# Optimization experiments

Hardware: AMD Instinct MI355X
Metric: run time of the kernel (lower is better)

The kernel has to match this reference:

```python
import jax, jax.numpy as jnp
import numpy as np

N_UNITS = 1024
D_K = 64
B, S = 4, 2048
NEG = 1.0e9


def setup_inputs() -> dict:
    key = jax.random.key(0)
    ks = jax.random.split(key, 11)
    k = float(np.sqrt(1.0 / N_UNITS))
    u = lambda kk, shape: jax.random.uniform(kk, shape, jnp.float32, -k, k)
    Q = jax.random.normal(ks[0], (B, S, N_UNITS), jnp.float32)
    K = jax.random.normal(ks[1], (B, S, N_UNITS), jnp.float32)
    V = jax.random.normal(ks[2], (B, S, N_UNITS), jnp.float32)
    mask = jax.random.randint(ks[3], (B, S, S), 0, 2, jnp.int32)
    return {
        "Q": Q, "K": K, "V": V, "mask": mask,
        "Wq_w": u(ks[4], (D_K, N_UNITS)), "Wq_b": u(ks[5], (D_K,)),
        "Wk_w": u(ks[6], (D_K, N_UNITS)), "Wk_b": u(ks[7], (D_K,)),
        "Wv_w": u(ks[8], (D_K, N_UNITS)), "Wv_b": u(ks[9], (D_K,)),
    }


def reference(Q, K, V, mask, Wq_w, Wq_b, Wk_w, Wk_b, Wv_w, Wv_b):
    # Linear projections (torch Linear: x @ W.T + b)
    Q_ = jnp.einsum('bsu,du->bsd', Q, Wq_w) + Wq_b  # [B,S,D_K]
    K_ = jnp.einsum('bsu,du->bsd', K, Wk_w) + Wk_b
    V_ = jnp.einsum('bsu,du->bsd', V, Wv_w) + Wv_b
    scores = jnp.einsum('bid,bjd->bij', Q_, K_) / jnp.sqrt(jnp.float32(D_K))
    m = mask.astype(jnp.float32)
    # custom multiplicative-additive mask: scores*mask - 1e9*(1-mask)
    masked = scores * m - NEG * (1.0 - m)
    attn = jax.nn.softmax(masked, axis=-1)
    # dropout p=0.0 -> identity
    return jnp.einsum('bij,bjd->bid', attn, V_)
```

## Files before the change

kernel.cpp:

```cpp
#include <hip/hip_runtime.h>
#include <stdint.h>

#define S_ 2048

typedef __bf16 bf16x8 __attribute__((ext_vector_type(8)));
typedef float f32x4 __attribute__((ext_vector_type(4)));
typedef unsigned int u32x4 __attribute__((ext_vector_type(4)));

union FragU { u32x4 u; bf16x8 v; unsigned short s[8]; };

__device__ __forceinline__ unsigned short f2bf(float f) {
    unsigned int u = __builtin_bit_cast(unsigned int, f);
    u += 0x7fffu + ((u >> 16) & 1u);
    return (unsigned short)(u >> 16);
}
__device__ __forceinline__ unsigned int pk2(float a, float b) {
    return (unsigned int)f2bf(a) | ((unsigned int)f2bf(b) << 16);
}
__device__ __forceinline__ void gl_lds16(const void* g, void* l) {
    __builtin_amdgcn_global_load_lds(
        (const __attribute__((address_space(1))) unsigned int*)g,
        (__attribute__((address_space(3))) unsigned int*)l, 16, 0, 0);
}

__global__ __launch_bounds__(256) void cvt_w_kernel(
    const float* __restrict__ wq, const float* __restrict__ wk,
    const float* __restrict__ wv, u32x4* __restrict__ Wt4)
{
    const int lane = threadIdx.x & 63;
    const int lm = lane & 15, quad = lane >> 4;
    const int f = blockIdx.x * 4 + (threadIdx.x >> 6);
    const int mat = f >> 7, cg = (f >> 5) & 3, s = f & 31;
    const float* W = (mat == 0) ? wq : (mat == 1) ? wk : wv;
    const float* src = W + (cg * 16 + lm) * 1024 + s * 32 + quad * 8;
    float4 a = *(const float4*)(src);
    float4 b = *(const float4*)(src + 4);
    FragU o;
    o.u[0] = pk2(a.x, a.y); o.u[1] = pk2(a.z, a.w);
    o.u[2] = pk2(b.x, b.y); o.u[3] = pk2(b.z, b.w);
    Wt4[f * 64 + lane] = o.u;
}

__global__ __launch_bounds__(256, 2) void proj_mask_kernel(
    const float* __restrict__ Q, const float* __restrict__ K, const float* __restrict__ V,
    const u32x4* __restrict__ Wt4,
    const float* __restrict__ Bq, const float* __restrict__ Bk, const float* __restrict__ Bv,
    const int* __restrict__ mask,
    unsigned short* __restrict__ Qb, unsigned short* __restrict__ Kb,
    unsigned short* __restrict__ Vf,
    unsigned long long* __restrict__ bits)
{
    const int tid = threadIdx.x;
    const int w = tid >> 6, lane = tid & 63;
    const int g = blockIdx.x / 7, j = blockIdx.x % 7;

    __shared__ __align__(16) float Xs[16][1028];

    if (j >= 3) {
        const int wid = (g * 4 + (j - 3)) * 4 + w;
        const int* p = mask + wid * 2048 + lane;
        int mm[32];
        #pragma unroll
        for (int t = 0; t < 32; ++t) mm[t] = p[t * 64];
        #pragma unroll
        for (int t = 0; t < 32; ++t) {
            unsigned long long bb = __ballot(mm[t] != 0);
            if (lane == 0) bits[wid * 32 + t] = bb;
        }
        return;
    }

    const int lm = lane & 15, quad = lane >> 4;
    const int mat = j;
    const int row0 = g * 16;

    const float* X    = (mat == 0) ? Q  : (mat == 1) ? K  : V;
    const float* Bias = (mat == 0) ? Bq : (mat == 1) ? Bk : Bv;

    #pragma unroll
    for (int i = 0; i < 16; ++i) {
        const int r = w * 4 + (i >> 2);
        const int qd = i & 3;
        gl_lds16(X + (row0 + r) * 1024 + qd * 256 + lane * 4, &Xs[r][qd * 256]);
    }
    __syncthreads();

    f32x4 acc = {0.f, 0.f, 0.f, 0.f};
    const u32x4* wfrag = Wt4 + (mat * 128 + w * 32) * 64 + lane;
    #pragma unroll 8
    for (int s = 0; s < 32; ++s) {
        f32x4 a0 = *(const f32x4*)&Xs[lm][s * 32 + quad * 8];
        f32x4 a1 = *(const f32x4*)&Xs[lm][s * 32 + quad * 8 + 4];
        FragU af, bfr;
        af.u[0] = pk2(a0[0], a0[1]); af.u[1] = pk2(a0[2], a0[3]);
        af.u[2] = pk2(a1[0], a1[1]); af.u[3] = pk2(a1[2], a1[3]);
        bfr.u = wfrag[s * 64];
        acc = __builtin_amdgcn_mfma_f32_16x16x32_bf16(af.v, bfr.v, acc, 0, 0, 0);
    }

    const int col = w * 16 + lm;
    const float bias = Bias[col];
    if (mat == 2) {
        const int seq0 = row0 + quad * 4;
        const int b_ = seq0 >> 11;
        const int s = seq0 & 2047;
        const int sb = s >> 5, s32 = s & 31;
        const int fq = s32 >> 3, j0 = s32 & 7;
        ushort4 vv;
        unsigned short* vs = (unsigned short*)&vv;
        #pragma unroll
        for (int r = 0; r < 4; ++r) vs[r] = f2bf(acc[r] + bias);
        char* dst = (char*)Vf + ((b_ * 64 + sb) * 4 + w) * 1024
                    + (fq * 16 + lm) * 16 + j0 * 2;
        *(ushort4*)dst = vv;
    } else {
        unsigned short* dst = (mat == 0) ? Qb : Kb;
        #pragma unroll
        for (int r = 0; r < 4; ++r)
            dst[(row0 + quad * 4 + r) * 64 + col] = f2bf(acc[r] + bias);
    }
}

__global__ __launch_bounds__(512) void attn_kernel(
    const unsigned short* __restrict__ Qb, const unsigned short* __restrict__ Kb,
    const u32x4* __restrict__ Vf4, const unsigned long long* __restrict__ bits,
    float* __restrict__ out)
{
    const int tid = threadIdx.x;
    const int w = tid >> 6, lane = tid & 63;
    const int lm = lane & 15, quad = lane >> 4;
    const int q0 = blockIdx.x * 16;
    const int b = blockIdx.y;

    __shared__ unsigned long long Mb[16][32];
    __shared__ unsigned short Plds[8][16 * 72];
    __shared__ float Olds[8][1024];
    __shared__ float llds[8][16];

    {
        const int p = tid >> 5, kw = tid & 31;
        Mb[p][kw] = bits[(b * 2048 + q0 + p) * 32 + kw];
    }

    FragU qf0, qf1;
    const unsigned short* qptr = Qb + (b * 2048 + q0 + lm) * 64 + quad * 8;
    qf0.u = *(const u32x4*)qptr;
    qf1.u = *(const u32x4*)(qptr + 32);

    f32x4 o[4];
    #pragma unroll
    for (int dt = 0; dt < 4; ++dt) { f32x4 z = {0.f,0.f,0.f,0.f}; o[dt] = z; }
    float lsum[4] = {0.f, 0.f, 0.f, 0.f};

    const unsigned short* kbase = Kb + b * 2048 * 64;
    const u32x4* vbase = Vf4 + (b * 64) * 4 * 64;

    __syncthreads();

    #pragma unroll
    for (int iter = 0; iter < 4; ++iter) {
        const int k0 = w * 256 + iter * 64;
        const int kw = k0 >> 6;

        f32x4 sc[4];
        #pragma unroll
        for (int ct = 0; ct < 4; ++ct) {
            const unsigned short* kptr = kbase + (k0 + ct * 16 + lm) * 64 + quad * 8;
            FragU kf0, kf1;
            kf0.u = *(const u32x4*)kptr;
            kf1.u = *(const u32x4*)(kptr + 32);
            f32x4 a = {0.f,0.f,0.f,0.f};
            a = __builtin_amdgcn_mfma_f32_16x16x32_bf16(qf0.v, kf0.v, a, 0, 0, 0);
            a = __builtin_amdgcn_mfma_f32_16x16x32_bf16(qf1.v, kf1.v, a, 0, 0, 0);
            sc[ct] = a;
        }

        unsigned long long mb[4];
        #pragma unroll
        for (int r = 0; r < 4; ++r) mb[r] = Mb[quad * 4 + r][kw];

        #pragma unroll
        for (int ct = 0; ct < 4; ++ct) {
            #pragma unroll
            for (int r = 0; r < 4; ++r) {
                float p = ((mb[r] >> (ct * 16 + lm)) & 1ull)
                          ? __expf(sc[ct][r] * 0.125f) : 0.f;
                sc[ct][r] = p;
                lsum[r] += p;
            }
        }

        #pragma unroll
        for (int ct = 0; ct < 4; ++ct)
            #pragma unroll
            for (int r = 0; r < 4; ++r)
                Plds[w][(quad * 4 + r) * 72 + ct * 16 + lm] = f2bf(sc[ct][r]);

        #pragma unroll
        for (int ks = 0; ks < 2; ++ks) {
            FragU pf;
            pf.u = *(const u32x4*)&Plds[w][lm * 72 + ks * 32 + quad * 8];
            const int sb = (k0 >> 5) + ks;
            #pragma unroll
            for (int dt = 0; dt < 4; ++dt) {
                FragU vf;
                vf.u = vbase[(sb * 4 + dt) * 64 + lane];
                o[dt] = __builtin_amdgcn_mfma_f32_16x16x32_bf16(pf.v, vf.v, o[dt], 0, 0, 0);
            }
        }
    }

    #pragma unroll
    for (int r = 0; r < 4; ++r)
        #pragma unroll
        for (int off = 1; off <= 8; off <<= 1)
            lsum[r] += __shfl_xor(lsum[r], off, 64);

    #pragma unroll
    for (int dt = 0; dt < 4; ++dt)
        #pragma unroll
        for (int r = 0; r < 4; ++r)
            Olds[w][(quad * 4 + r) * 64 + dt * 16 + lm] = o[dt][r];
    if (lm == 0)
        #pragma unroll
        for (int r = 0; r < 4; ++r) llds[w][quad * 4 + r] = lsum[r];
    __syncthreads();

    #pragma unroll
    for (int i = 0; i < 2; ++i) {
        int e = i * 512 + tid;
        int q = e >> 6, d = e & 63;
        float L = 0.f, val = 0.f;
        #pragma unroll
        for (int ww = 0; ww < 8; ++ww) {
            L   += llds[ww][q];
            val += Olds[ww][q * 64 + d];
        }
        out[(b * 2048 + q0 + q) * 64 + d] = val / L;
    }
}

extern "C" void kernel_launch(void* const* d_in, const int* in_sizes, int n_in,
                              void* d_out, int out_size, void* d_ws, size_t ws_size,
                              hipStream_t stream) {
    const float* Q   = (const float*)d_in[0];
    const float* K   = (const float*)d_in[1];
    const float* V   = (const float*)d_in[2];
    const int* mask  = (const int*)d_in[3];
    const float* Wq  = (const float*)d_in[4];
    const float* bq  = (const float*)d_in[5];
    const float* Wk  = (const float*)d_in[6];
    const float* bk  = (const float*)d_in[7];
    const float* Wv  = (const float*)d_in[8];
    const float* bv  = (const float*)d_in[9];
    float* out = (float*)d_out;

    char* ws = (char*)d_ws;
    unsigned short* Qb = (unsigned short*)(ws);
    unsigned short* Kb = (unsigned short*)(ws + (1u << 20));
    unsigned short* Vf = (unsigned short*)(ws + (2u << 20));
    u32x4* Wt4 = (u32x4*)(ws + (3u << 20));
    unsigned long long* bits = (unsigned long long*)(ws + (4u << 20));

    hipLaunchKernelGGL(cvt_w_kernel, dim3(96), dim3(256), 0, stream, Wq, Wk, Wv, Wt4);
    hipLaunchKernelGGL(proj_mask_kernel, dim3(3584), dim3(256), 0, stream,
                       Q, K, V, Wt4, bq, bk, bv, mask, Qb, Kb, Vf, bits);
    hipLaunchKernelGGL(attn_kernel, dim3(128, 4), dim3(512), 0, stream,
                       Qb, Kb, (const u32x4*)Vf, bits, out);
}
```

Before: 215.1 us.

## Store K in MFMA fragment layout and process 32 queries per attention block

The projection kernel now writes K directly in the per-lane MFMA fragment order, so the attention kernel fetches each K fragment with one coalesced 16-byte load per lane instead of strided row loads. The attention kernel now handles 32 query rows per block, with waves split into two query groups and four key groups, each covering 512 keys. Each loaded K/V tile now serves two query tiles across the block, and the grid is halved. In exchange there are fewer blocks (256) and a longer per-wave loop, which may reduce latency hiding.

```diff
diff --git a/kernel.cpp b/kernel.cpp
--- a/kernel.cpp
+++ b/kernel.cpp
@@ -46,7 +46,7 @@
     const u32x4* __restrict__ Wt4,
     const float* __restrict__ Bq, const float* __restrict__ Bk, const float* __restrict__ Bv,
     const int* __restrict__ mask,
-    unsigned short* __restrict__ Qb, unsigned short* __restrict__ Kb,
+    unsigned short* __restrict__ Qb, unsigned short* __restrict__ Kf,
     unsigned short* __restrict__ Vf,
     unsigned long long* __restrict__ bits)
 {
@@ -100,7 +100,17 @@
 
     const int col = w * 16 + lm;
     const float bias = Bias[col];
-    if (mat == 2) {
+    if (mat == 0) {
+        #pragma unroll
+        for (int r = 0; r < 4; ++r)
+            Qb[(row0 + quad * 4 + r) * 64 + col] = f2bf(acc[r] + bias);
+    } else if (mat == 1) {
+        const int qp = (w & 1) * 2 + (lm >> 3);
+        unsigned short* base = Kf + ((unsigned)(g * 2 + (w >> 1)) * 64 + qp * 16 + quad * 4) * 8 + (lm & 7);
+        #pragma unroll
+        for (int r = 0; r < 4; ++r)
+            base[r * 8] = f2bf(acc[r] + bias);
+    } else {
         const int seq0 = row0 + quad * 4;
         const int b_ = seq0 >> 11;
         const int s = seq0 & 2047;
@@ -113,37 +123,36 @@
         char* dst = (char*)Vf + ((b_ * 64 + sb) * 4 + w) * 1024
                     + (fq * 16 + lm) * 16 + j0 * 2;
         *(ushort4*)dst = vv;
-    } else {
-        unsigned short* dst = (mat == 0) ? Qb : Kb;
-        #pragma unroll
-        for (int r = 0; r < 4; ++r)
-            dst[(row0 + quad * 4 + r) * 64 + col] = f2bf(acc[r] + bias);
     }
 }
 
 __global__ __launch_bounds__(512) void attn_kernel(
-    const unsigned short* __restrict__ Qb, const unsigned short* __restrict__ Kb,
+    const unsigned short* __restrict__ Qb, const u32x4* __restrict__ Kf4,
     const u32x4* __restrict__ Vf4, const unsigned long long* __restrict__ bits,
     float* __restrict__ out)
 {
     const int tid = threadIdx.x;
     const int w = tid >> 6, lane = tid & 63;
     const int lm = lane & 15, quad = lane >> 4;
-    const int q0 = blockIdx.x * 16;
+    const int qg = w & 1, kg = w >> 1;
+    const int q0 = blockIdx.x * 32;
     const int b = blockIdx.y;
 
-    __shared__ unsigned long long Mb[16][32];
+    __shared__ unsigned long long Mb[32][32];
     __shared__ unsigned short Plds[8][16 * 72];
-    __shared__ float Olds[8][1024];
-    __shared__ float llds[8][16];
+    __shared__ float Olds[4][32 * 64];
+    __shared__ float llds[4][32];
 
     {
-        const int p = tid >> 5, kw = tid & 31;
-        Mb[p][kw] = bits[(b * 2048 + q0 + p) * 32 + kw];
+        const int e0 = tid * 2;
+        const int p = e0 >> 5, kw = e0 & 31;
+        const unsigned long long* src = bits + (b * 2048 + q0 + p) * 32 + kw;
+        Mb[p][kw] = src[0];
+        Mb[p][kw + 1] = src[1];
     }
 
     FragU qf0, qf1;
-    const unsigned short* qptr = Qb + (b * 2048 + q0 + lm) * 64 + quad * 8;
+    const unsigned short* qptr = Qb + (b * 2048 + q0 + qg * 16 + lm) * 64 + quad * 8;
     qf0.u = *(const u32x4*)qptr;
     qf1.u = *(const u32x4*)(qptr + 32);
 
@@ -152,23 +161,23 @@
     for (int dt = 0; dt < 4; ++dt) { f32x4 z = {0.f,0.f,0.f,0.f}; o[dt] = z; }
     float lsum[4] = {0.f, 0.f, 0.f, 0.f};
 
-    const unsigned short* kbase = Kb + b * 2048 * 64;
+    const u32x4* kfb = Kf4 + (b * 128) * 2 * 64;
     const u32x4* vbase = Vf4 + (b * 64) * 4 * 64;
 
     __syncthreads();
 
-    #pragma unroll
-    for (int iter = 0; iter < 4; ++iter) {
-        const int k0 = w * 256 + iter * 64;
-        const int kw = k0 >> 6;
+    #pragma unroll 4
+    for (int iter = 0; iter < 8; ++iter) {
+        const int k0 = kg * 512 + iter * 64;
+        const int kw = kg * 8 + iter;
 
         f32x4 sc[4];
         #pragma unroll
         for (int ct = 0; ct < 4; ++ct) {
-            const unsigned short* kptr = kbase + (k0 + ct * 16 + lm) * 64 + quad * 8;
+            const int kt = (k0 >> 4) + ct;
             FragU kf0, kf1;
-            kf0.u = *(const u32x4*)kptr;
-            kf1.u = *(const u32x4*)(kptr + 32);
+            kf0.u = kfb[(kt * 2 + 0) * 64 + lane];
+            kf1.u = kfb[(kt * 2 + 1) * 64 + lane];
             f32x4 a = {0.f,0.f,0.f,0.f};
             a = __builtin_amdgcn_mfma_f32_16x16x32_bf16(qf0.v, kf0.v, a, 0, 0, 0);
             a = __builtin_amdgcn_mfma_f32_16x16x32_bf16(qf1.v, kf1.v, a, 0, 0, 0);
@@ -177,7 +186,7 @@
 
         unsigned long long mb[4];
         #pragma unroll
-        for (int r = 0; r < 4; ++r) mb[r] = Mb[quad * 4 + r][kw];
+        for (int r = 0; r < 4; ++r) mb[r] = Mb[qg * 16 + quad * 4 + r][kw];
 
         #pragma unroll
         for (int ct = 0; ct < 4; ++ct) {
@@ -220,21 +229,21 @@
     for (int dt = 0; dt < 4; ++dt)
         #pragma unroll
         for (int r = 0; r < 4; ++r)
-            Olds[w][(quad * 4 + r) * 64 + dt * 16 + lm] = o[dt][r];
+            Olds[kg][(qg * 16 + quad * 4 + r) * 64 + dt * 16 + lm] = o[dt][r];
     if (lm == 0)
         #pragma unroll
-        for (int r = 0; r < 4; ++r) llds[w][quad * 4 + r] = lsum[r];
+        for (int r = 0; r < 4; ++r) llds[kg][qg * 16 + quad * 4 + r] = lsum[r];
     __syncthreads();
 
     #pragma unroll
-    for (int i = 0; i < 2; ++i) {
+    for (int i = 0; i < 4; ++i) {
         int e = i * 512 + tid;
         int q = e >> 6, d = e & 63;
         float L = 0.f, val = 0.f;
         #pragma unroll
-        for (int ww = 0; ww < 8; ++ww) {
-            L   += llds[ww][q];
-            val += Olds[ww][q * 64 + d];
+        for (int kk = 0; kk < 4; ++kk) {
+            L   += llds[kk][q];
+            val += Olds[kk][q * 64 + d];
         }
         out[(b * 2048 + q0 + q) * 64 + d] = val / L;
     }
@@ -257,14 +266,14 @@
 
     char* ws = (char*)d_ws;
     unsigned short* Qb = (unsigned short*)(ws);
-    unsigned short* Kb = (unsigned short*)(ws + (1u << 20));
+    unsigned short* Kf = (unsigned short*)(ws + (1u << 20));
     unsigned short* Vf = (unsigned short*)(ws + (2u << 20));
     u32x4* Wt4 = (u32x4*)(ws + (3u << 20));
     unsigned long long* bits = (unsigned long long*)(ws + (4u << 20));
 
     hipLaunchKernelGGL(cvt_w_kernel, dim3(96), dim3(256), 0, stream, Wq, Wk, Wv, Wt4);
     hipLaunchKernelGGL(proj_mask_kernel, dim3(3584), dim3(256), 0, stream,
-                       Q, K, V, Wt4, bq, bk, bv, mask, Qb, Kb, Vf, bits);
-    hipLaunchKernelGGL(attn_kernel, dim3(128, 4), dim3(512), 0, stream,
-                       Qb, Kb, (const u32x4*)Vf, bits, out);
-}
+                       Q, K, V, Wt4, bq, bk, bv, mask, Qb, Kf, Vf, bits);
+    hipLaunchKernelGGL(attn_kernel, dim3(64, 4), dim3(512), 0, stream,
+                       Qb, (const u32x4*)Kf, (const u32x4*)Vf, bits, out);
+}
```

Result: no change. 218.4 us (+1.6%).
